# Performance work log

Hardware: AMD Instinct MI355X
Metric: run time of the kernel (lower is better)

The kernel has to match this reference:

```python
import jax, jax.numpy as jnp
import numpy as np


def setup_inputs() -> dict:
    key = jax.random.key(0)
    B, S, H, D = 4, 2048, 16, 64
    kq, kk, kv, kl = jax.random.split(key, 4)
    q = jax.random.normal(kq, (B, S, H, D), dtype=jnp.float32)
    k = jax.random.normal(kk, (B, S, H, D), dtype=jnp.float32)
    v = jax.random.normal(kv, (B, S, H, D), dtype=jnp.float32)
    # varlen: each sequence has a valid prefix length in [S//2, S]
    lengths = jax.random.randint(kl, (B,), S // 2, S + 1)
    key_padding_mask = jnp.arange(S)[None, :] < lengths[:, None]  # [B, S] bool
    return {"q": q, "k": k, "v": v, "key_padding_mask": key_padding_mask}


def reference(q, k, v, key_padding_mask):
    # q,k,v: [B, S, H, D]; key_padding_mask: [B, S] (True = valid key/value token).
    # Equivalent math of ring varlen flash attention: every query attends to all
    # valid (unpadded) key positions of its sequence; padded keys are excluded.
    D = q.shape[-1]
    scale = 1.0 / np.sqrt(D).astype(np.float32)
    scores = jnp.einsum('bshd,bthd->bhst', q, k) * scale  # [B, H, S, S]
    neg = jnp.finfo(scores.dtype).min
    scores = jnp.where(key_padding_mask[:, None, None, :], scores, neg)
    probs = jax.nn.softmax(scores, axis=-1)
    context = jnp.einsum('bhst,bthd->bshd', probs, v)  # [B, S, H, D]
    return context
```

## Files before the change

### kernel.cpp

```cpp
#include <hip/hip_runtime.h>

#define BB 4
#define SS 2048
#define HH 16
#define DD 64

#define NQW 8
#define QW  32
#define QB  (NQW*QW)
#define KVB 32

#define KRS 144
#define VRS 80

typedef short bf16x8 __attribute__((ext_vector_type(8)));
typedef float f32x16 __attribute__((ext_vector_type(16)));

__device__ __forceinline__ unsigned cvtpk(float lo, float hi){
    unsigned r;
    asm("v_cvt_pk_bf16_f32 %0, %1, %2" : "=v"(r) : "v"(lo), "v"(hi));
    return r;
}

#if __has_builtin(__builtin_amdgcn_exp2f)
#define EXP2F(x) __builtin_amdgcn_exp2f(x)
#else
__device__ __forceinline__ float exp2_asm(float x){
    float r; asm("v_exp_f32 %0, %1\n\ts_nop 0" : "=v"(r) : "v"(x)); return r;
}
#define EXP2F(x) exp2_asm(x)
#endif

union FragU { unsigned u[4]; bf16x8 v; };

#if __has_builtin(__builtin_amdgcn_permlane32_swap)
__device__ __forceinline__ void plswap(unsigned &a, unsigned &b, int ){
    auto r = __builtin_amdgcn_permlane32_swap(a, b, false, false);
    a = r[0]; b = r[1];
}
#else
__device__ __forceinline__ void plswap(unsigned &a, unsigned &b, int lh){
    unsigned sb = (unsigned)__shfl_xor((int)b, 32);
    unsigned sa = (unsigned)__shfl_xor((int)a, 32);
    unsigned na = lh ? sb : a;
    unsigned nb = lh ? b  : sa;
    a = na; b = nb;
}
#endif

__global__ __launch_bounds__(512)
void attn_mfma(const float* __restrict__ qg, const float* __restrict__ kg,
               const float* __restrict__ vg, const int* __restrict__ maskg,
               float* __restrict__ outg)
{
    __shared__ __align__(16) unsigned char kl_raw[2][KVB*KRS];
    __shared__ __align__(16) unsigned char vt_raw[2][DD*VRS];
    __shared__ int lsum_s[NQW];

    const int i0 = (int)blockIdx.x;
    const int x  = i0 & 7;
    const int j  = i0 >> 3;
    const int qt = j & 7;
    const int g  = j >> 3;
    const int b  = (x + g) & 3;
    const int h  = (g << 1) | (x >> 2);

    const int t    = (int)threadIdx.x;
    const int wid  = t >> 6;
    const int lane = t & 63;
    const int lq   = lane & 31;
    const int lh   = lane >> 5;

    const int* mrow = maskg + b*SS;
    int part = 0;
    #pragma unroll
    for (int i = 0; i < 4; ++i) part += mrow[t*4 + i];
    #pragma unroll
    for (int off = 1; off < 64; off <<= 1) part += __shfl_xor(part, off);
    if (lane == 0) lsum_s[wid] = part;
    __syncthreads();
    int L = 0;
    #pragma unroll
    for (int w = 0; w < NQW; ++w) L += lsum_s[w];
    const int nt = (L + KVB - 1) / KVB;

    const int q0 = qt*QB + wid*QW + lq;
    const float* qrow = qg + ((size_t)((size_t)b*SS + q0)*HH + h)*DD;
    const float QSC = 0.125f * 1.44269504088896340736f;
    bf16x8 Qh[4];
    #pragma unroll
    for (int kc = 0; kc < 4; ++kc) {
        const float* p = qrow + kc*16 + lh*8;
        float4 a = *(const float4*)p;
        float4 c4 = *(const float4*)(p + 4);
        FragU f;
        f.u[0] = cvtpk(a.x*QSC, a.y*QSC);
        f.u[1] = cvtpk(a.z*QSC, a.w*QSC);
        f.u[2] = cvtpk(c4.x*QSC, c4.y*QSC);
        f.u[3] = cvtpk(c4.z*QSC, c4.w*QSC);
        Qh[kc] = f.v;
    }

    f32x16 O0, O1, ZERO;
    #pragma unroll
    for (int i = 0; i < 16; ++i) { O0[i] = 0.f; O1[i] = 0.f; ZERO[i] = 0.f; }
    float lp = 0.f;

    const size_t kvstride = (size_t)HH*DD;
    const float* kbase = kg + ((size_t)b*SS*HH + h)*(size_t)DD;
    const float* vbase = vg + ((size_t)b*SS*HH + h)*(size_t)DD;

    const int skr  = t >> 4;
    const int sc4  = (t & 15) * 4;
    const int skp  = t & 15;
    const int d0v  = (t >> 4) * 2;

    float kx[4], va_[2], vb_[2];

    auto LOADT = [&](int kt0) {
        const float* kp = kbase + (size_t)(kt0 + skr)*kvstride + sc4;
        float4 a = *(const float4*)kp;
        kx[0]=a.x; kx[1]=a.y; kx[2]=a.z; kx[3]=a.w;
        const float* vp0 = vbase + (size_t)(kt0 + 2*skp)*kvstride + d0v;
        const float* vp1 = vp0 + kvstride;
        float2 d2 = *(const float2*)vp0;
        float2 e2 = *(const float2*)vp1;
        va_[0]=d2.x; va_[1]=d2.y;
        vb_[0]=e2.x; vb_[1]=e2.y;
    };

    auto CVTW = [&](int bsel) {
        uint2 kf;
        kf.x = cvtpk(kx[0], kx[1]);
        kf.y = cvtpk(kx[2], kx[3]);
        unsigned koff = (unsigned)skr*KRS + (unsigned)sc4*2u;
        koff ^= ((unsigned)(skr>>3)&3u) << 4;
        *(uint2*)(kl_raw[bsel] + koff) = kf;
        #pragma unroll
        for (int i2 = 0; i2 < 2; ++i2) {
            unsigned dw = cvtpk(va_[i2], vb_[i2]);
            *(unsigned*)(vt_raw[bsel] + (unsigned)(d0v + i2)*VRS + (unsigned)skp*4u) = dw;
        }
    };

    LOADT(0);
    CVTW(0);

    for (int it = 0; it < nt; ++it) {
        __syncthreads();
        const int  cur  = it & 1;
        const bool more = (it + 1 < nt);
        if (more) LOADT((it + 1) * KVB);

        const unsigned char* klb = kl_raw[cur];
        __builtin_amdgcn_s_setprio(1);
        FragU kf0;
        {
            unsigned off = (unsigned)lq*KRS + (unsigned)(lh*16);
            off ^= ((unsigned)(lq>>3)&3u) << 4;
            kf0.v = *(const bf16x8*)(klb + off);
        }
        f32x16 S = __builtin_amdgcn_mfma_f32_32x32x16_bf16(kf0.v, Qh[0], ZERO, 0, 0, 0);
        #pragma unroll
        for (int kc = 1; kc < 4; ++kc) {
            unsigned off = (unsigned)lq*KRS + (unsigned)(kc*32 + lh*16);
            off ^= ((unsigned)(lq>>3)&3u) << 4;
            FragU kf;
            kf.v = *(const bf16x8*)(klb + off);
            S = __builtin_amdgcn_mfma_f32_32x32x16_bf16(kf.v, Qh[kc], S, 0, 0, 0);
        }
        __builtin_amdgcn_s_setprio(0);

        const int kt0 = it * KVB;
        if (kt0 + KVB > L) {
            #pragma unroll
            for (int r = 0; r < 16; ++r) {
                const int key = kt0 + (r&3) + 8*(r>>2) + 4*lh;
                if (key >= L) S[r] = -1e30f;
            }
        }

        float p[16];
        #pragma unroll
        for (int r = 0; r < 16; ++r) p[r] = EXP2F(S[r]);

        float s0 = (p[0] + p[1]) + (p[2] + p[3]);
        float s1 = (p[4] + p[5]) + (p[6] + p[7]);
        float s2 = (p[8] + p[9]) + (p[10] + p[11]);
        float s3 = (p[12] + p[13]) + (p[14] + p[15]);
        lp += (s0 + s1) + (s2 + s3);

        unsigned dw[8];
        #pragma unroll
        for (int jj = 0; jj < 8; ++jj) dw[jj] = cvtpk(p[2*jj], p[2*jj+1]);
        plswap(dw[0], dw[2], lh);  plswap(dw[1], dw[3], lh);
        plswap(dw[4], dw[6], lh);  plswap(dw[5], dw[7], lh);
        FragU B0, B1;
        B0.u[0]=dw[0]; B0.u[1]=dw[1]; B0.u[2]=dw[2]; B0.u[3]=dw[3];
        B1.u[0]=dw[4]; B1.u[1]=dw[5]; B1.u[2]=dw[6]; B1.u[3]=dw[7];

        const unsigned char* vtb = vt_raw[cur];
        __builtin_amdgcn_s_setprio(1);
        #pragma unroll
        for (int kc = 0; kc < 2; ++kc) {
            const unsigned ko = (unsigned)(kc*32 + lh*16);
            FragU vva, vvb;
            vva.v = *(const bf16x8*)(vtb + (unsigned)lq*VRS + ko);
            vvb.v = *(const bf16x8*)(vtb + (unsigned)(lq+32)*VRS + ko);
            O0 = __builtin_amdgcn_mfma_f32_32x32x16_bf16(vva.v, kc ? B1.v : B0.v, O0, 0, 0, 0);
            O1 = __builtin_amdgcn_mfma_f32_32x32x16_bf16(vvb.v, kc ? B1.v : B0.v, O1, 0, 0, 0);
        }
        __builtin_amdgcn_s_setprio(0);

        if (more) CVTW(cur ^ 1);
    }

    lp += __shfl_xor(lp, 32);
    const float inv = 1.0f / lp;
    float* orow = outg + ((size_t)((size_t)b*SS + q0)*HH + h)*DD;
    #pragma unroll
    for (int run = 0; run < 4; ++run) {
        float4 w0, w1;
        w0.x = O0[4*run+0]*inv; w0.y = O0[4*run+1]*inv;
        w0.z = O0[4*run+2]*inv; w0.w = O0[4*run+3]*inv;
        w1.x = O1[4*run+0]*inv; w1.y = O1[4*run+1]*inv;
        w1.z = O1[4*run+2]*inv; w1.w = O1[4*run+3]*inv;
        *(float4*)(orow + 8*run + 4*lh)      = w0;
        *(float4*)(orow + 32 + 8*run + 4*lh) = w1;
    }
}

extern "C" void kernel_launch(void* const* d_in, const int* in_sizes, int n_in,
                              void* d_out, int out_size, void* d_ws, size_t ws_size,
                              hipStream_t stream) {
    const float* q    = (const float*)d_in[0];
    const float* k    = (const float*)d_in[1];
    const float* v    = (const float*)d_in[2];
    const int*   mask = (const int*)d_in[3];
    float* out = (float*)d_out;

    dim3 grid(BB * HH * (SS / QB));
    dim3 block(512);
    hipLaunchKernelGGL(attn_mfma, grid, block, 0, stream, q, k, v, mask, out);
}
```

Measured before the change: 78.13 us.

## Permute K rows in LDS to drop permlane swaps and sum denominator via MFMA

K rows are written to LDS in a permuted order so the QK^T accumulator layout lines up with the PV B-operand layout. That removes the permlane32 swaps after the bf16 conversion. The softmax row sum is now taken with an extra MFMA against a vector of bf16 ones rather than with VALU adds and a cross-half shuffle. This cuts VALU and cross-lane work per tile but adds a third PV-stage MFMA per kc step, and the denominator is now summed from bf16-rounded probabilities.

After: 80.67 us. 1.03x slower.

```diff
diff --git a/kernel.cpp b/kernel.cpp
--- a/kernel.cpp
+++ b/kernel.cpp
@@ -32,21 +32,6 @@
 #endif
 
 union FragU { unsigned u[4]; bf16x8 v; };
-
-#if __has_builtin(__builtin_amdgcn_permlane32_swap)
-__device__ __forceinline__ void plswap(unsigned &a, unsigned &b, int ){
-    auto r = __builtin_amdgcn_permlane32_swap(a, b, false, false);
-    a = r[0]; b = r[1];
-}
-#else
-__device__ __forceinline__ void plswap(unsigned &a, unsigned &b, int lh){
-    unsigned sb = (unsigned)__shfl_xor((int)b, 32);
-    unsigned sa = (unsigned)__shfl_xor((int)a, 32);
-    unsigned na = lh ? sb : a;
-    unsigned nb = lh ? b  : sa;
-    a = na; b = nb;
-}
-#endif
 
 __global__ __launch_bounds__(512)
 void attn_mfma(const float* __restrict__ qg, const float* __restrict__ kg,
@@ -101,10 +86,13 @@
         Qh[kc] = f.v;
     }
 
-    f32x16 O0, O1, ZERO;
-    #pragma unroll
-    for (int i = 0; i < 16; ++i) { O0[i] = 0.f; O1[i] = 0.f; ZERO[i] = 0.f; }
-    float lp = 0.f;
+    FragU ones;
+    ones.u[0] = 0x3f803f80u; ones.u[1] = 0x3f803f80u;
+    ones.u[2] = 0x3f803f80u; ones.u[3] = 0x3f803f80u;
+
+    f32x16 O0, O1, Osum, ZERO;
+    #pragma unroll
+    for (int i = 0; i < 16; ++i) { O0[i]=0.f; O1[i]=0.f; Osum[i]=0.f; ZERO[i]=0.f; }
 
     const size_t kvstride = (size_t)HH*DD;
     const float* kbase = kg + ((size_t)b*SS*HH + h)*(size_t)DD;
@@ -112,6 +100,8 @@
 
     const int skr  = t >> 4;
     const int sc4  = (t & 15) * 4;
+    const int blkp = ((skr >> 2) ^ (skr >> 3)) & 1;
+    const int pskr = skr ^ (blkp ? 12 : 0);
     const int skp  = t & 15;
     const int d0v  = (t >> 4) * 2;
 
@@ -133,8 +123,8 @@
         uint2 kf;
         kf.x = cvtpk(kx[0], kx[1]);
         kf.y = cvtpk(kx[2], kx[3]);
-        unsigned koff = (unsigned)skr*KRS + (unsigned)sc4*2u;
-        koff ^= ((unsigned)(skr>>3)&3u) << 4;
+        unsigned koff = (unsigned)pskr*KRS + (unsigned)sc4*2u;
+        koff ^= ((unsigned)(pskr>>3)&3u) << 4;
         *(uint2*)(kl_raw[bsel] + koff) = kf;
         #pragma unroll
         for (int i2 = 0; i2 < 2; ++i2) {
@@ -175,7 +165,7 @@
         if (kt0 + KVB > L) {
             #pragma unroll
             for (int r = 0; r < 16; ++r) {
-                const int key = kt0 + (r&3) + 8*(r>>2) + 4*lh;
+                const int key = kt0 + r + 8*(r>>3) + 8*lh;
                 if (key >= L) S[r] = -1e30f;
             }
         }
@@ -184,20 +174,11 @@
         #pragma unroll
         for (int r = 0; r < 16; ++r) p[r] = EXP2F(S[r]);
 
-        float s0 = (p[0] + p[1]) + (p[2] + p[3]);
-        float s1 = (p[4] + p[5]) + (p[6] + p[7]);
-        float s2 = (p[8] + p[9]) + (p[10] + p[11]);
-        float s3 = (p[12] + p[13]) + (p[14] + p[15]);
-        lp += (s0 + s1) + (s2 + s3);
-
-        unsigned dw[8];
-        #pragma unroll
-        for (int jj = 0; jj < 8; ++jj) dw[jj] = cvtpk(p[2*jj], p[2*jj+1]);
-        plswap(dw[0], dw[2], lh);  plswap(dw[1], dw[3], lh);
-        plswap(dw[4], dw[6], lh);  plswap(dw[5], dw[7], lh);
         FragU B0, B1;
-        B0.u[0]=dw[0]; B0.u[1]=dw[1]; B0.u[2]=dw[2]; B0.u[3]=dw[3];
-        B1.u[0]=dw[4]; B1.u[1]=dw[5]; B1.u[2]=dw[6]; B1.u[3]=dw[7];
+        B0.u[0] = cvtpk(p[0],  p[1]);  B0.u[1] = cvtpk(p[2],  p[3]);
+        B0.u[2] = cvtpk(p[4],  p[5]);  B0.u[3] = cvtpk(p[6],  p[7]);
+        B1.u[0] = cvtpk(p[8],  p[9]);  B1.u[1] = cvtpk(p[10], p[11]);
+        B1.u[2] = cvtpk(p[12], p[13]); B1.u[3] = cvtpk(p[14], p[15]);
 
         const unsigned char* vtb = vt_raw[cur];
         __builtin_amdgcn_s_setprio(1);
@@ -207,16 +188,17 @@
             FragU vva, vvb;
             vva.v = *(const bf16x8*)(vtb + (unsigned)lq*VRS + ko);
             vvb.v = *(const bf16x8*)(vtb + (unsigned)(lq+32)*VRS + ko);
-            O0 = __builtin_amdgcn_mfma_f32_32x32x16_bf16(vva.v, kc ? B1.v : B0.v, O0, 0, 0, 0);
-            O1 = __builtin_amdgcn_mfma_f32_32x32x16_bf16(vvb.v, kc ? B1.v : B0.v, O1, 0, 0, 0);
+            const bf16x8 Bk = kc ? B1.v : B0.v;
+            O0   = __builtin_amdgcn_mfma_f32_32x32x16_bf16(vva.v,  Bk, O0,   0, 0, 0);
+            O1   = __builtin_amdgcn_mfma_f32_32x32x16_bf16(vvb.v,  Bk, O1,   0, 0, 0);
+            Osum = __builtin_amdgcn_mfma_f32_32x32x16_bf16(ones.v, Bk, Osum, 0, 0, 0);
         }
         __builtin_amdgcn_s_setprio(0);
 
         if (more) CVTW(cur ^ 1);
     }
 
-    lp += __shfl_xor(lp, 32);
-    const float inv = 1.0f / lp;
+    const float inv = 1.0f / Osum[0];
     float* orow = outg + ((size_t)((size_t)b*SS + q0)*HH + h)*DD;
     #pragma unroll
     for (int run = 0; run < 4; ++run) {
```
